# Optimization experiments

Hardware: AMD Instinct MI355X
Metric: run time of the kernel (lower is better)

Reference implementation:

```python
import jax, jax.numpy as jnp
import numpy as np

INPUT_DIM = 1024
OUTPUT_DIM = 1024
SPLINE_POINTS = 4

def setup_inputs() -> dict:
    key = jax.random.key(0)
    k1, k2 = jax.random.split(key)
    x = jax.random.normal(k1, (4096, INPUT_DIM), dtype=jnp.float32)
    spline_coeffs = jax.random.normal(k2, (OUTPUT_DIM, INPUT_DIM, SPLINE_POINTS, 4), dtype=jnp.float32)
    return {"x": x, "spline_coeffs": spline_coeffs}

def reference(x, spline_coeffs):
    # Per-feature min-max normalization over the batch dim (as in the torch code,
    # where x[:, j].min()/max() are taken over the batch).
    xmin = jnp.min(x, axis=0, keepdims=True)   # [1, D]
    xmax = jnp.max(x, axis=0, keepdims=True)
    xn = (x - xmin) / (xmax - xmin)            # [B, D]

    # The original sums the cubic polynomial over all spline_points, so the
    # effective coefficients are the sum over the spline_points axis.
    c = jnp.sum(spline_coeffs, axis=2)         # [O, D, 4]

    x2 = xn * xn
    x3 = x2 * xn
    # out[b, o] = sum_d c0*x^3 + c1*x^2 + c2*x + c3
    out = (jnp.einsum('bd,od->bo', x3, c[..., 0])
           + jnp.einsum('bd,od->bo', x2, c[..., 1])
           + jnp.einsum('bd,od->bo', xn, c[..., 2])
           + jnp.sum(c[..., 3], axis=1)[None, :])
    return out
```

## Files before the change

### kernel.cpp

```cpp
#include <hip/hip_runtime.h>
#include <hip/hip_bf16.h>
#include <stdint.h>
#include <stddef.h>

typedef __bf16 bf16;
typedef __attribute__((ext_vector_type(4))) __bf16 bf16x4;
typedef __attribute__((ext_vector_type(8))) __bf16 bf16x8;
typedef __attribute__((ext_vector_type(4))) float f32x4;

#define BATCH 4096
#define DIM 1024
#define ODIM 1024
#define K3 3072

#define WS_P      0
#define WS_CB     25165824
#define WS_BIAS   31457280
#define WS_PMIN   31461376
#define WS_PMAX   32509952
#define WS_MINV   33558528
#define WS_SCALE  33562624

#define ASYNC16(g, l)                                                          \
  __builtin_amdgcn_global_load_lds(                                            \
      (__attribute__((address_space(1))) void*)(g),                            \
      (__attribute__((address_space(3))) void*)(l), 16, 0, 0)

#define WAIT_VM(n) __builtin_amdgcn_s_waitcnt(0x0F00 | 0x0070 | ((n)&15) | ((((n)>>4)&3)<<14))
#define BARRIER()                     \
  do {                                \
    asm volatile("" ::: "memory");    \
    __builtin_amdgcn_s_barrier();     \
    asm volatile("" ::: "memory");    \
  } while (0)

__global__ void k_stream(const float* __restrict__ x,
                         float* __restrict__ pmin,
                         float* __restrict__ pmax,
                         const float* __restrict__ sp,
                         bf16* __restrict__ CB,
                         float* __restrict__ bias) {
  __shared__ float red[4];
  const int t = threadIdx.x;
  if (blockIdx.x < 256) {
    const int ch = blockIdx.x;
    const float* p = x + (size_t)ch * 16 * DIM + (t << 2);
    f32x4 mn = {1e30f, 1e30f, 1e30f, 1e30f};
    f32x4 mx = {-1e30f, -1e30f, -1e30f, -1e30f};
#pragma unroll
    for (int r = 0; r < 16; ++r) {
      f32x4 v = *(const f32x4*)(p + (size_t)r * DIM);
#pragma unroll
      for (int j = 0; j < 4; ++j) {
        mn[j] = fminf(mn[j], v[j]);
        mx[j] = fmaxf(mx[j], v[j]);
      }
    }
    *(f32x4*)(pmin + ch * DIM + (t << 2)) = mn;
    *(f32x4*)(pmax + ch * DIM + (t << 2)) = mx;
  } else {
    const int o = blockIdx.x - 256;
    const int d = t << 2;
    f32x4 s[4];
#pragma unroll
    for (int dd = 0; dd < 4; ++dd) {
      const float* p = sp + ((size_t)o * DIM + d + dd) * 16;
      f32x4 acc = *(const f32x4*)(p);
      acc += *(const f32x4*)(p + 4);
      acc += *(const f32x4*)(p + 8);
      acc += *(const f32x4*)(p + 12);
      s[dd] = acc;
    }
    size_t cb = (size_t)o * K3 + d;
    bf16x4 c0 = {(bf16)s[0][0], (bf16)s[1][0], (bf16)s[2][0], (bf16)s[3][0]};
    bf16x4 c1 = {(bf16)s[0][1], (bf16)s[1][1], (bf16)s[2][1], (bf16)s[3][1]};
    bf16x4 c2 = {(bf16)s[0][2], (bf16)s[1][2], (bf16)s[2][2], (bf16)s[3][2]};
    *(bf16x4*)(CB + cb) = c0;
    *(bf16x4*)(CB + cb + 1024) = c1;
    *(bf16x4*)(CB + cb + 2048) = c2;
    float v = s[0][3] + s[1][3] + s[2][3] + s[3][3];
#pragma unroll
    for (int off = 32; off > 0; off >>= 1) v += __shfl_down(v, off, 64);
    int lane = t & 63, w = t >> 6;
    if (lane == 0) red[w] = v;
    __syncthreads();
    if (t == 0) bias[o] = red[0] + red[1] + red[2] + red[3];
  }
}

__global__ void k_minmax_final(const float* __restrict__ pmin,
                               const float* __restrict__ pmax,
                               float* __restrict__ minv,
                               float* __restrict__ scale) {
  __shared__ float smn[4][64], smx[4][64];
  const int t = threadIdx.x;
  const int lane = t & 63;
  const int w = t >> 6;
  const int col = blockIdx.x * 64 + lane;
  float mn = 1e30f, mx = -1e30f;
#pragma unroll 8
  for (int ch = w; ch < 256; ch += 4) {
    mn = fminf(mn, pmin[ch * DIM + col]);
    mx = fmaxf(mx, pmax[ch * DIM + col]);
  }
  smn[w][lane] = mn;
  smx[w][lane] = mx;
  __syncthreads();
  if (w == 0) {
    mn = fminf(fminf(smn[0][lane], smn[1][lane]), fminf(smn[2][lane], smn[3][lane]));
    mx = fmaxf(fmaxf(smx[0][lane], smx[1][lane]), fmaxf(smx[2][lane], smx[3][lane]));
    minv[col] = mn;
    scale[col] = 1.0f / (mx - mn);
  }
}

__global__ void k_powers(const float* __restrict__ x,
                         const float* __restrict__ minv,
                         const float* __restrict__ scale,
                         bf16* __restrict__ P) {
  const int t = threadIdx.x;
  const int b = blockIdx.x * 2 + (t >> 7);
  const int d = (t & 127) << 3;
  f32x4 xv0 = *(const f32x4*)(x + (size_t)b * DIM + d);
  f32x4 xv1 = *(const f32x4*)(x + (size_t)b * DIM + d + 4);
  f32x4 mn0 = *(const f32x4*)(minv + d);
  f32x4 mn1 = *(const f32x4*)(minv + d + 4);
  f32x4 sc0 = *(const f32x4*)(scale + d);
  f32x4 sc1 = *(const f32x4*)(scale + d + 4);
  bf16x8 o3, o2, o1;
#pragma unroll
  for (int j = 0; j < 4; ++j) {
    float xn = (xv0[j] - mn0[j]) * sc0[j];
    float x2 = xn * xn;
    float x3 = x2 * xn;
    o3[j] = (bf16)x3;
    o2[j] = (bf16)x2;
    o1[j] = (bf16)xn;
    float yn = (xv1[j] - mn1[j]) * sc1[j];
    float y2 = yn * yn;
    float y3 = y2 * yn;
    o3[j + 4] = (bf16)y3;
    o2[j + 4] = (bf16)y2;
    o1[j + 4] = (bf16)yn;
  }
  size_t base = (size_t)b * K3 + d;
  *(bf16x8*)(P + base) = o3;
  *(bf16x8*)(P + base + 1024) = o2;
  *(bf16x8*)(P + base + 2048) = o1;
}

#define BM 128
#define BN 128
#define BKE 64
#define NIT (K3 / BKE)
#define NBUF 3
__global__ __launch_bounds__(512, 2) void k_gemm(const bf16* __restrict__ P,
                                                 const bf16* __restrict__ CBm,
                                                 const float* __restrict__ bias,
                                                 float* __restrict__ out) {
  __shared__ bf16 ldsm[NBUF][2][BM * BKE];

  const int tid = threadIdx.x;
  const int wave = tid >> 6;
  const int lane = tid & 63;

  const int f = blockIdx.x;
  const int chunk = f & 7;
  const int idx = f >> 3;
  const int mt = ((chunk >> 1) << 3) + (idx >> 2);
  const int nt = ((chunk & 1) << 2) + (idx & 3);
  const int bm = mt * BM;
  const int bn = nt * BN;

  const int wr = (wave >> 2) * 64;
  const int wc = (wave & 3) * 32;

  const size_t rowbytes = (size_t)K3 * 2;

  const char* gAp[2];
  const char* gBp[2];
  int ldso[2];
#pragma unroll
  for (int i = 0; i < 2; ++i) {
    int off = i * 8192 + tid * 16;
    int row = off >> 7;
    int q = (off >> 4) & 7;
    int gb = (q ^ (row & 7)) * 16;
    gAp[i] = (const char*)P + (size_t)(bm + row) * rowbytes + gb;
    gBp[i] = (const char*)CBm + (size_t)(bn + row) * rowbytes + gb;
    ldso[i] = i * 8192 + wave * 1024;
  }

  f32x4 acc[4][2] = {};

  const int mrow = lane & 15;
  const int kq = lane >> 4;

#define STAGE(buf, kt)                                                        \
  do {                                                                        \
    const size_t kb_ = (size_t)(kt) * (BKE * 2);                              \
    char* lA_ = (char*)&ldsm[buf][0][0];                                      \
    char* lB_ = (char*)&ldsm[buf][1][0];                                      \
    _Pragma("unroll") for (int i_ = 0; i_ < 2; ++i_)                          \
        ASYNC16(gAp[i_] + kb_, lA_ + ldso[i_]);                               \
    _Pragma("unroll") for (int i_ = 0; i_ < 2; ++i_)                          \
        ASYNC16(gBp[i_] + kb_, lB_ + ldso[i_]);                               \
  } while (0)

#define COMPUTE(buf)                                                          \
  do {                                                                        \
    const bf16* sA_ = &ldsm[buf][0][0];                                       \
    const bf16* sB_ = &ldsm[buf][1][0];                                       \
    _Pragma("unroll") for (int ks = 0; ks < 2; ++ks) {                        \
      bf16x8 af[4], bg[2];                                                    \
      _Pragma("unroll") for (int i = 0; i < 4; ++i) {                         \
        int row = wr + i * 16 + mrow;                                         \
        int sq = (ks * 4 + kq) ^ (row & 7);                                   \
        af[i] = *(const bf16x8*)&sA_[row * BKE + sq * 8];                     \
      }                                                                       \
      _Pragma("unroll") for (int j = 0; j < 2; ++j) {                         \
        int row = wc + j * 16 + mrow;                                         \
        int sq = (ks * 4 + kq) ^ (row & 7);                                   \
        bg[j] = *(const bf16x8*)&sB_[row * BKE + sq * 8];                     \
      }                                                                       \
      _Pragma("unroll") for (int i = 0; i < 4; ++i)                           \
          _Pragma("unroll") for (int j = 0; j < 2; ++j)                       \
              acc[i][j] = __builtin_amdgcn_mfma_f32_16x16x32_bf16(            \
                  af[i], bg[j], acc[i][j], 0, 0, 0);                          \
    }                                                                         \
  } while (0)

  STAGE(0, 0);
  STAGE(1, 1);
#pragma unroll 3
  for (int kt = 0; kt < NIT - 2; ++kt) {
    STAGE((kt + 2) % NBUF, kt + 2);
    WAIT_VM(8);
    BARRIER();
    COMPUTE(kt % NBUF);
    BARRIER();
  }
  WAIT_VM(4);
  BARRIER();
  COMPUTE((NIT - 2) % NBUF);
  BARRIER();
  WAIT_VM(0);
  BARRIER();
  COMPUTE((NIT - 1) % NBUF);

  const int ccol = lane & 15;
  const int crow = (lane >> 4) * 4;
#pragma unroll
  for (int j = 0; j < 2; ++j) {
    const int col = bn + wc + j * 16 + ccol;
    const float bv = bias[col];
#pragma unroll
    for (int i = 0; i < 4; ++i) {
      const int row0 = bm + wr + i * 16 + crow;
#pragma unroll
      for (int r = 0; r < 4; ++r)
        out[(size_t)(row0 + r) * ODIM + col] = acc[i][j][r] + bv;
    }
  }
#undef STAGE
#undef COMPUTE
}

extern "C" void kernel_launch(void* const* d_in, const int* in_sizes, int n_in,
                              void* d_out, int out_size, void* d_ws, size_t ws_size,
                              hipStream_t stream) {
  (void)in_sizes; (void)n_in; (void)out_size; (void)ws_size;
  const float* x = (const float*)d_in[0];
  const float* sp = (const float*)d_in[1];
  float* out = (float*)d_out;
  char* ws = (char*)d_ws;

  bf16* Pm = (bf16*)(ws + WS_P);
  bf16* CBm = (bf16*)(ws + WS_CB);
  float* bias = (float*)(ws + WS_BIAS);
  float* pmin = (float*)(ws + WS_PMIN);
  float* pmax = (float*)(ws + WS_PMAX);
  float* minv = (float*)(ws + WS_MINV);
  float* scale = (float*)(ws + WS_SCALE);

  k_stream<<<1280, 256, 0, stream>>>(x, pmin, pmax, sp, CBm, bias);
  k_minmax_final<<<16, 256, 0, stream>>>(pmin, pmax, minv, scale);
  k_powers<<<2048, 256, 0, stream>>>(x, minv, scale, Pm);
  k_gemm<<<256, 512, 0, stream>>>(Pm, CBm, bias, out);
}
```

Measured before the change: 152.4 us.

## Fuse power computation into GEMM, building the A tile in LDS from x

Removes the separate k_powers kernel and the bf16 power-matrix workspace. The GEMM now loads raw x rows, normalises them with min/scale values cached in LDS, and writes the x^3/x^2/x bf16 tiles into a double-buffered swizzled LDS buffer. The B coefficients are read straight from global memory into registers instead of through async LDS staging. This cuts the large power-matrix write and re-read and one kernel launch. In exchange the B loads are no longer prefetched, so their latency sits in the inner loop, and the bigger shared-memory footprint may reduce blocks per CU.

Result: slower. 173.7 us (+14.0%).

```diff
diff --git a/kernel.cpp b/kernel.cpp
--- a/kernel.cpp
+++ b/kernel.cpp
@@ -13,26 +13,20 @@
 #define ODIM 1024
 #define K3 3072
 
-#define WS_P      0
-#define WS_CB     25165824
-#define WS_BIAS   31457280
-#define WS_PMIN   31461376
-#define WS_PMAX   32509952
-#define WS_MINV   33558528
-#define WS_SCALE  33562624
-
-#define ASYNC16(g, l)                                                          \
-  __builtin_amdgcn_global_load_lds(                                            \
-      (__attribute__((address_space(1))) void*)(g),                            \
-      (__attribute__((address_space(3))) void*)(l), 16, 0, 0)
-
-#define WAIT_VM(n) __builtin_amdgcn_s_waitcnt(0x0F00 | 0x0070 | ((n)&15) | ((((n)>>4)&3)<<14))
+#define WS_CB     0
+#define WS_BIAS   6291456
+#define WS_PMIN   6295552
+#define WS_PMAX   7344128
+#define WS_MINV   8392704
+#define WS_SCALE  8396800
+
 #define BARRIER()                     \
   do {                                \
     asm volatile("" ::: "memory");    \
     __builtin_amdgcn_s_barrier();     \
     asm volatile("" ::: "memory");    \
   } while (0)
+#define WAIT_LGKM() __builtin_amdgcn_s_waitcnt(0xC07F)
 
 __global__ void k_stream(const float* __restrict__ x,
                          float* __restrict__ pmin,
@@ -114,51 +108,15 @@
   }
 }
 
-__global__ void k_powers(const float* __restrict__ x,
-                         const float* __restrict__ minv,
-                         const float* __restrict__ scale,
-                         bf16* __restrict__ P) {
-  const int t = threadIdx.x;
-  const int b = blockIdx.x * 2 + (t >> 7);
-  const int d = (t & 127) << 3;
-  f32x4 xv0 = *(const f32x4*)(x + (size_t)b * DIM + d);
-  f32x4 xv1 = *(const f32x4*)(x + (size_t)b * DIM + d + 4);
-  f32x4 mn0 = *(const f32x4*)(minv + d);
-  f32x4 mn1 = *(const f32x4*)(minv + d + 4);
-  f32x4 sc0 = *(const f32x4*)(scale + d);
-  f32x4 sc1 = *(const f32x4*)(scale + d + 4);
-  bf16x8 o3, o2, o1;
-#pragma unroll
-  for (int j = 0; j < 4; ++j) {
-    float xn = (xv0[j] - mn0[j]) * sc0[j];
-    float x2 = xn * xn;
-    float x3 = x2 * xn;
-    o3[j] = (bf16)x3;
-    o2[j] = (bf16)x2;
-    o1[j] = (bf16)xn;
-    float yn = (xv1[j] - mn1[j]) * sc1[j];
-    float y2 = yn * yn;
-    float y3 = y2 * yn;
-    o3[j + 4] = (bf16)y3;
-    o2[j + 4] = (bf16)y2;
-    o1[j + 4] = (bf16)yn;
-  }
-  size_t base = (size_t)b * K3 + d;
-  *(bf16x8*)(P + base) = o3;
-  *(bf16x8*)(P + base + 1024) = o2;
-  *(bf16x8*)(P + base + 2048) = o1;
-}
-
-#define BM 128
-#define BN 128
-#define BKE 64
-#define NIT (K3 / BKE)
-#define NBUF 3
-__global__ __launch_bounds__(512, 2) void k_gemm(const bf16* __restrict__ P,
+#define MSOFF 98304
+#define ABUF(b) ((b) * 49152)
+__global__ __launch_bounds__(512, 2) void k_gemm(const float* __restrict__ x,
+                                                 const float* __restrict__ minv,
+                                                 const float* __restrict__ scale,
                                                  const bf16* __restrict__ CBm,
                                                  const float* __restrict__ bias,
                                                  float* __restrict__ out) {
-  __shared__ bf16 ldsm[NBUF][2][BM * BKE];
+  __shared__ __attribute__((aligned(16))) char smem[106496];
 
   const int tid = threadIdx.x;
   const int wave = tid >> 6;
@@ -169,84 +127,111 @@
   const int idx = f >> 3;
   const int mt = ((chunk >> 1) << 3) + (idx >> 2);
   const int nt = ((chunk & 1) << 2) + (idx & 3);
-  const int bm = mt * BM;
-  const int bn = nt * BN;
+  const int bm = mt * 128;
+  const int bn = nt * 128;
 
   const int wr = (wave >> 2) * 64;
   const int wc = (wave & 3) * 32;
-
-  const size_t rowbytes = (size_t)K3 * 2;
-
-  const char* gAp[2];
-  const char* gBp[2];
-  int ldso[2];
-#pragma unroll
-  for (int i = 0; i < 2; ++i) {
-    int off = i * 8192 + tid * 16;
-    int row = off >> 7;
-    int q = (off >> 4) & 7;
-    int gb = (q ^ (row & 7)) * 16;
-    gAp[i] = (const char*)P + (size_t)(bm + row) * rowbytes + gb;
-    gBp[i] = (const char*)CBm + (size_t)(bn + row) * rowbytes + gb;
-    ldso[i] = i * 8192 + wave * 1024;
-  }
-
-  f32x4 acc[4][2] = {};
-
   const int mrow = lane & 15;
   const int kq = lane >> 4;
 
-#define STAGE(buf, kt)                                                        \
+  const int prow = tid >> 2;
+  const int cq = tid & 3;
+  const int c0 = cq << 4;
+  const int s0 = (((cq << 1)) ^ (prow & 7)) << 4;
+  const int s1 = (((cq << 1) | 1) ^ (prow & 7)) << 4;
+
+  const float* xg = x + (size_t)(bm + prow) * DIM + c0;
+
+  if (tid < 256) {
+    f32x4 m = *(const f32x4*)(minv + tid * 4);
+    *(f32x4*)(smem + MSOFF + tid * 16) = m;
+  } else {
+    f32x4 s = *(const f32x4*)(scale + (tid - 256) * 4);
+    *(f32x4*)(smem + MSOFF + 4096 + (tid - 256) * 16) = s;
+  }
+
+  f32x4 xv0, xv1, xv2, xv3;
+#define LOADX(dtv)                                                            \
   do {                                                                        \
-    const size_t kb_ = (size_t)(kt) * (BKE * 2);                              \
-    char* lA_ = (char*)&ldsm[buf][0][0];                                      \
-    char* lB_ = (char*)&ldsm[buf][1][0];                                      \
-    _Pragma("unroll") for (int i_ = 0; i_ < 2; ++i_)                          \
-        ASYNC16(gAp[i_] + kb_, lA_ + ldso[i_]);                               \
-    _Pragma("unroll") for (int i_ = 0; i_ < 2; ++i_)                          \
-        ASYNC16(gBp[i_] + kb_, lB_ + ldso[i_]);                               \
-  } while (0)
-
-#define COMPUTE(buf)                                                          \
+    const float* xp_ = xg + (dtv) * 64;                                       \
+    xv0 = *(const f32x4*)(xp_);                                               \
+    xv1 = *(const f32x4*)(xp_ + 4);                                           \
+    xv2 = *(const f32x4*)(xp_ + 8);                                           \
+    xv3 = *(const f32x4*)(xp_ + 12);                                          \
+  } while (0)
+
+#define POWERS_WRITE(abuf, dtv)                                               \
   do {                                                                        \
-    const bf16* sA_ = &ldsm[buf][0][0];                                       \
-    const bf16* sB_ = &ldsm[buf][1][0];                                       \
-    _Pragma("unroll") for (int ks = 0; ks < 2; ++ks) {                        \
-      bf16x8 af[4], bg[2];                                                    \
-      _Pragma("unroll") for (int i = 0; i < 4; ++i) {                         \
-        int row = wr + i * 16 + mrow;                                         \
-        int sq = (ks * 4 + kq) ^ (row & 7);                                   \
-        af[i] = *(const bf16x8*)&sA_[row * BKE + sq * 8];                     \
+    const char* ms_ = smem + MSOFF + ((dtv) * 64 + c0) * 4;                   \
+    f32x4 xn0 = (xv0 - *(const f32x4*)(ms_)) * *(const f32x4*)(ms_ + 4096);   \
+    f32x4 xn1 = (xv1 - *(const f32x4*)(ms_ + 16)) * *(const f32x4*)(ms_ + 4112); \
+    f32x4 xn2 = (xv2 - *(const f32x4*)(ms_ + 32)) * *(const f32x4*)(ms_ + 4128); \
+    f32x4 xn3 = (xv3 - *(const f32x4*)(ms_ + 48)) * *(const f32x4*)(ms_ + 4144); \
+    f32x4 x20 = xn0 * xn0, x21 = xn1 * xn1, x22 = xn2 * xn2, x23 = xn3 * xn3; \
+    f32x4 x30 = x20 * xn0, x31 = x21 * xn1, x32 = x22 * xn2, x33 = x23 * xn3; \
+    bf16x8 w3lo, w3hi, w2lo, w2hi, w1lo, w1hi;                                \
+    _Pragma("unroll") for (int e = 0; e < 4; ++e) {                           \
+      w3lo[e] = (bf16)x30[e]; w3lo[e + 4] = (bf16)x31[e];                     \
+      w3hi[e] = (bf16)x32[e]; w3hi[e + 4] = (bf16)x33[e];                     \
+      w2lo[e] = (bf16)x20[e]; w2lo[e + 4] = (bf16)x21[e];                     \
+      w2hi[e] = (bf16)x22[e]; w2hi[e + 4] = (bf16)x23[e];                     \
+      w1lo[e] = (bf16)xn0[e]; w1lo[e + 4] = (bf16)xn1[e];                     \
+      w1hi[e] = (bf16)xn2[e]; w1hi[e + 4] = (bf16)xn3[e];                     \
+    }                                                                         \
+    char* aw_ = smem + ABUF(abuf) + prow * 128;                               \
+    *(bf16x8*)(aw_ + s0) = w3lo;                                              \
+    *(bf16x8*)(aw_ + s1) = w3hi;                                              \
+    *(bf16x8*)(aw_ + 16384 + s0) = w2lo;                                      \
+    *(bf16x8*)(aw_ + 16384 + s1) = w2hi;                                      \
+    *(bf16x8*)(aw_ + 32768 + s0) = w1lo;                                      \
+    *(bf16x8*)(aw_ + 32768 + s1) = w1hi;                                      \
+  } while (0)
+
+  f32x4 acc[4][2] = {};
+  const char* cbT = (const char*)CBm + (size_t)(bn + wc + mrow) * 6144 + kq * 16;
+
+#define COMPUTE(abuf, dtv)                                                    \
+  do {                                                                        \
+    _Pragma("unroll") for (int p = 0; p < 3; ++p) {                           \
+      const char* cb_ = cbT + p * 2048 + (dtv) * 128;                         \
+      bf16x8 bg[2][2];                                                        \
+      _Pragma("unroll") for (int j = 0; j < 2; ++j)                           \
+        _Pragma("unroll") for (int ks = 0; ks < 2; ++ks)                      \
+            bg[j][ks] = *(const bf16x8*)(cb_ + (size_t)j * 16 * 6144 + ks * 64); \
+      const char* ab_ = smem + ABUF(abuf) + p * 16384;                        \
+      _Pragma("unroll") for (int ks = 0; ks < 2; ++ks) {                      \
+        bf16x8 af[4];                                                         \
+        _Pragma("unroll") for (int i = 0; i < 4; ++i) {                       \
+          int row_ = wr + i * 16 + mrow;                                      \
+          int su_ = ((ks * 4 + kq) ^ (row_ & 7)) * 16;                        \
+          af[i] = *(const bf16x8*)(ab_ + row_ * 128 + su_);                   \
+        }                                                                     \
+        _Pragma("unroll") for (int i = 0; i < 4; ++i)                         \
+            _Pragma("unroll") for (int j = 0; j < 2; ++j)                     \
+                acc[i][j] = __builtin_amdgcn_mfma_f32_16x16x32_bf16(          \
+                    af[i], bg[j][ks], acc[i][j], 0, 0, 0);                    \
       }                                                                       \
-      _Pragma("unroll") for (int j = 0; j < 2; ++j) {                         \
-        int row = wc + j * 16 + mrow;                                         \
-        int sq = (ks * 4 + kq) ^ (row & 7);                                   \
-        bg[j] = *(const bf16x8*)&sB_[row * BKE + sq * 8];                     \
-      }                                                                       \
-      _Pragma("unroll") for (int i = 0; i < 4; ++i)                           \
-          _Pragma("unroll") for (int j = 0; j < 2; ++j)                       \
-              acc[i][j] = __builtin_amdgcn_mfma_f32_16x16x32_bf16(            \
-                  af[i], bg[j], acc[i][j], 0, 0, 0);                          \
     }                                                                         \
   } while (0)
 
-  STAGE(0, 0);
-  STAGE(1, 1);
-#pragma unroll 3
-  for (int kt = 0; kt < NIT - 2; ++kt) {
-    STAGE((kt + 2) % NBUF, kt + 2);
-    WAIT_VM(8);
+  LOADX(0);
+  WAIT_LGKM();
+  BARRIER();
+  POWERS_WRITE(0, 0);
+  LOADX(1);
+  WAIT_LGKM();
+  BARRIER();
+
+#pragma unroll 2
+  for (int dt = 0; dt < 15; ++dt) {
+    COMPUTE(dt & 1, dt);
+    POWERS_WRITE((dt + 1) & 1, dt + 1);
+    if (dt < 14) LOADX(dt + 2);
+    WAIT_LGKM();
     BARRIER();
-    COMPUTE(kt % NBUF);
-    BARRIER();
-  }
-  WAIT_VM(4);
-  BARRIER();
-  COMPUTE((NIT - 2) % NBUF);
-  BARRIER();
-  WAIT_VM(0);
-  BARRIER();
-  COMPUTE((NIT - 1) % NBUF);
+  }
+  COMPUTE(1, 15);
 
   const int ccol = lane & 15;
   const int crow = (lane >> 4) * 4;
@@ -262,7 +247,8 @@
         out[(size_t)(row0 + r) * ODIM + col] = acc[i][j][r] + bv;
     }
   }
-#undef STAGE
+#undef LOADX
+#undef POWERS_WRITE
 #undef COMPUTE
 }
 
@@ -275,7 +261,6 @@
   float* out = (float*)d_out;
   char* ws = (char*)d_ws;
 
-  bf16* Pm = (bf16*)(ws + WS_P);
   bf16* CBm = (bf16*)(ws + WS_CB);
   float* bias = (float*)(ws + WS_BIAS);
   float* pmin = (float*)(ws + WS_PMIN);
@@ -285,6 +270,5 @@
 
   k_stream<<<1280, 256, 0, stream>>>(x, pmin, pmax, sp, CBm, bias);
   k_minmax_final<<<16, 256, 0, stream>>>(pmin, pmax, minv, scale);
-  k_powers<<<2048, 256, 0, stream>>>(x, minv, scale, Pm);
-  k_gemm<<<256, 512, 0, stream>>>(Pm, CBm, bias, out);
-}
+  k_gemm<<<256, 512, 0, stream>>>(x, minv, scale, CBm, bias, out);
+}
```
